# Performance work log

Measured on AMD Instinct MI355X. Metric: run time of the kernel, lower is better.

## Reference

```python
import jax
import jax.numpy as jnp
from jax import lax
import numpy as np

N_PRE = 1024
N_POST = 2048
SEQ_LEN = 4096
DECAY = 0.9   # leak factor per timestep
V_TH = 1.0    # firing threshold


def setup_inputs() -> dict:
    key = jax.random.key(0)
    k1, k2 = jax.random.split(key)
    stim = (jax.random.uniform(k1, (N_PRE, SEQ_LEN), dtype=jnp.float32) < 0.1).astype(jnp.float32)  # sparse input spikes
    weights = jax.random.normal(k2, (N_POST, N_PRE), dtype=jnp.float32) * 0.05
    return {"stim": stim, "weights": weights}


def reference(stim, weights):
    # Synaptic currents for all timesteps at once: cal_post_input(stim[:, i]) == weights @ stim[:, i]
    currents = jnp.einsum("np,pt->nt", weights, stim)  # [n_post, T]

    def lif_step(v, i_t):
        # leaky integrate
        v = v * DECAY + i_t
        # fire
        s = (v >= V_TH).astype(v.dtype)
        # reset to 0 where spiked
        v_next = jnp.where(s > 0, jnp.zeros_like(v), v)
        return v_next, (s, v_next)

    v0 = jnp.zeros((N_POST,), dtype=stim.dtype)
    _, (spikes_t, v_t) = lax.scan(lif_step, v0, currents.T)  # scanned over T
    # transpose back to [n_post, T] to match spike_times / v buffers
    return spikes_t.T, v_t.T
```

## Files before the change

kernel.cpp:

```cpp
#include <hip/hip_runtime.h>

#define N_PRE 1024
#define N_POST 2048
#define SEQ_LEN 4096

#define KSPLIT 512

__device__ __forceinline__ float opaque(float x) {
  asm volatile("" : "+v"(x));
  return x;
}

__device__ __forceinline__ float load_dyn(const void* p, size_t idx, bool isbf) {
  if (isbf) {
    const unsigned short b = ((const unsigned short*)p)[idx];
    return __uint_as_float(((unsigned int)b) << 16);
  }
  return ((const float*)p)[idx];
}

__device__ __forceinline__ int sniff_flags(const void* W, const void* S, int tid,
                                           int* flags_sh) {
  if (tid < 64) {
    const unsigned short* uw = (const unsigned short*)W;
    const float f = fabsf(__uint_as_float(((unsigned int)uw[tid * 2]) << 16));
    const bool big = !(f < 64.f);
    const unsigned long long wb = __ballot(big);
    const unsigned short* us = (const unsigned short*)S;
    int hit = 0;
    for (int j = 0; j < 64; ++j) hit |= (us[tid * 128 + 2 * j] == 0x3F80u) ? 1 : 0;
    const unsigned long long sb = __ballot(hit != 0);
    if (tid == 0) *flags_sh = ((wb == 0ull) ? 1 : 0) | ((sb != 0ull) ? 2 : 0);
  }
  __syncthreads();
  return *flags_sh;
}

__global__ __launch_bounds__(256) void snn_wt_build(const void* __restrict__ W,
                                                    const void* __restrict__ S,
                                                    float* __restrict__ WT) {
  __shared__ float tile[64][65];
  __shared__ int flags_sh;
  const int tid = threadIdx.x;
  const int fl = sniff_flags(W, S, tid, &flags_sh);
  const bool w_bf = (fl & 1) != 0;
  const int k0 = blockIdx.x * 64;
  const int nn0 = blockIdx.y * 64;
  {
    const int r = tid >> 2;
    const int cq = tid & 3;
    if (!w_bf) {
      const float* Wf = (const float*)W;
#pragma unroll
      for (int p = 0; p < 4; ++p) {
        const int c = cq * 16 + p * 4;
        const float4 va = *(const float4*)&Wf[(size_t)(nn0 + r) * N_PRE + k0 + c];
        tile[c + 0][r] = va.x; tile[c + 1][r] = va.y;
        tile[c + 2][r] = va.z; tile[c + 3][r] = va.w;
      }
    } else {
#pragma unroll
      for (int p = 0; p < 4; ++p)
#pragma unroll
        for (int j = 0; j < 4; ++j) {
          const int c = cq * 16 + p * 4 + j;
          tile[c][r] = load_dyn(W, (size_t)(nn0 + r) * N_PRE + k0 + c, true);
        }
    }
  }
  __syncthreads();
  {
    const int kr = tid >> 2;
    const int nq = tid & 3;
#pragma unroll
    for (int p = 0; p < 4; ++p) {
      const int c = nq * 16 + p * 4;
      float4 o;
      o.x = tile[kr][c + 0]; o.y = tile[kr][c + 1];
      o.z = tile[kr][c + 2]; o.w = tile[kr][c + 3];
      *(float4*)&WT[(size_t)(k0 + kr) * N_POST + nn0 + c] = o;
    }
  }
}

__global__ __launch_bounds__(64) void snn_mask_build(const void* __restrict__ W,
                                                     const void* __restrict__ S,
                                                     unsigned char* __restrict__ MT) {
  __shared__ int flags_sh;
  const int tid = threadIdx.x;
  const int fl = sniff_flags(W, S, tid, &flags_sh);
  const bool s_bf = (fl & 2) != 0;
  const int tb = blockIdx.x;
  unsigned wrd[4] = {0u, 0u, 0u, 0u};
#pragma unroll
  for (int kk = 0; kk < 16; ++kk) {
    const int k = tid * 16 + kk;
    unsigned byte = 0;
    if (s_bf) {
      const unsigned short* Sb = (const unsigned short*)S;
      const uint4 u = *(const uint4*)&Sb[(size_t)k * SEQ_LEN + tb * 8];
      byte |= (((u.x & 0x7FFFu) != 0u) ? 1u : 0u) << 0;
      byte |= (((u.x & 0x7FFF0000u) != 0u) ? 1u : 0u) << 1;
      byte |= (((u.y & 0x7FFFu) != 0u) ? 1u : 0u) << 2;
      byte |= (((u.y & 0x7FFF0000u) != 0u) ? 1u : 0u) << 3;
      byte |= (((u.z & 0x7FFFu) != 0u) ? 1u : 0u) << 4;
      byte |= (((u.z & 0x7FFF0000u) != 0u) ? 1u : 0u) << 5;
      byte |= (((u.w & 0x7FFFu) != 0u) ? 1u : 0u) << 6;
      byte |= (((u.w & 0x7FFF0000u) != 0u) ? 1u : 0u) << 7;
    } else {
      const float* Sf = (const float*)S;
      const size_t base = (size_t)k * SEQ_LEN + tb * 8;
      const float4 f0 = *(const float4*)&Sf[base];
      const float4 f1 = *(const float4*)&Sf[base + 4];
      byte |= ((f0.x != 0.0f) ? 1u : 0u) << 0;
      byte |= ((f0.y != 0.0f) ? 1u : 0u) << 1;
      byte |= ((f0.z != 0.0f) ? 1u : 0u) << 2;
      byte |= ((f0.w != 0.0f) ? 1u : 0u) << 3;
      byte |= ((f1.x != 0.0f) ? 1u : 0u) << 4;
      byte |= ((f1.y != 0.0f) ? 1u : 0u) << 5;
      byte |= ((f1.z != 0.0f) ? 1u : 0u) << 6;
      byte |= ((f1.w != 0.0f) ? 1u : 0u) << 7;
    }
    wrd[kk >> 2] |= byte << ((kk & 3) * 8);
  }
  *(uint4*)&MT[(size_t)tb * N_PRE + tid * 16] =
      make_uint4(wrd[0], wrd[1], wrd[2], wrd[3]);
}

__global__ __launch_bounds__(64) void snn_list_build(const unsigned char* __restrict__ MT,
                                                     unsigned short* __restrict__ lists,
                                                     int* __restrict__ lens,
                                                     int* __restrict__ splits) {
  const int t = blockIdx.x;
  const int l = threadIdx.x;
  const unsigned char* Mrow = MT + (size_t)(t >> 3) * N_PRE;
  const int bit = t & 7;
  unsigned short* Lp = lists + (size_t)t * N_PRE;
  int base = 0;
  int split = 0;
#pragma unroll
  for (int c = 0; c < 16; ++c) {
    const int k = c * 64 + l;
    const int b = (Mrow[k] >> bit) & 1;
    const unsigned long long m = __ballot(b != 0);
    const int pre = __popcll(m & ((1ull << l) - 1ull));
    if (b) Lp[base + pre] = (unsigned short)k;
    base += __popcll(m);
    if (c == 7) split = base;
  }
  if (l == 0) {
    lens[t] = base;
    splits[t] = split;
  }
}

__global__ __launch_bounds__(64) void snn_gemm_sp(const float* __restrict__ WT,
                                                  const unsigned short* __restrict__ lists,
                                                  const int* __restrict__ lens,
                                                  float* __restrict__ C,
                                                  int t0, int ct) {
  const int slice = (int)blockIdx.x & 7;
  const int tl = (int)blockIdx.x >> 3;
  const int tg = t0 + tl;
  const int n = slice * 256 + (int)threadIdx.x * 4;
  const unsigned short* __restrict__ L = lists + (size_t)tg * N_PRE;
  const int len = lens[tg];
  float lo0 = 0.f, lo1 = 0.f, lo2 = 0.f, lo3 = 0.f;
  float hi0 = 0.f, hi1 = 0.f, hi2 = 0.f, hi3 = 0.f;

  int kA0, kA1, kA2, kA3, kA4, kA5, kA6, kA7;
  int kB0, kB1, kB2, kB3, kB4, kB5, kB6, kB7;
  float4 wA0, wA1, wA2, wA3, wA4, wA5, wA6, wA7;
  float4 wB0, wB1, wB2, wB3, wB4, wB5, wB6, wB7;

#define ISSUE(S, I)                                                    \
  {                                                                    \
    const uint4 u = *(const uint4*)&L[I];                              \
    k##S##0 = u.x & 0xFFFF; k##S##1 = (int)(u.x >> 16);                \
    k##S##2 = u.y & 0xFFFF; k##S##3 = (int)(u.y >> 16);                \
    k##S##4 = u.z & 0xFFFF; k##S##5 = (int)(u.z >> 16);                \
    k##S##6 = u.w & 0xFFFF; k##S##7 = (int)(u.w >> 16);                \
    w##S##0 = *(const float4*)&WT[((size_t)k##S##0 << 11) + n];        \
    w##S##1 = *(const float4*)&WT[((size_t)k##S##1 << 11) + n];        \
    w##S##2 = *(const float4*)&WT[((size_t)k##S##2 << 11) + n];        \
    w##S##3 = *(const float4*)&WT[((size_t)k##S##3 << 11) + n];        \
    w##S##4 = *(const float4*)&WT[((size_t)k##S##4 << 11) + n];        \
    w##S##5 = *(const float4*)&WT[((size_t)k##S##5 << 11) + n];        \
    w##S##6 = *(const float4*)&WT[((size_t)k##S##6 << 11) + n];        \
    w##S##7 = *(const float4*)&WT[((size_t)k##S##7 << 11) + n];        \
  }
#define ACC_LO(W_) { lo0 += W_.x; lo1 += W_.y; lo2 += W_.z; lo3 += W_.w; }
#define ACC_HI(W_) { hi0 += W_.x; hi1 += W_.y; hi2 += W_.z; hi3 += W_.w; }
#define ACC_SEL(K_, W_)                                                \
  { if ((K_) < KSPLIT) ACC_LO(W_) else ACC_HI(W_) }
#define ACCUM(S)                                                       \
  {                                                                    \
    if (k##S##7 < KSPLIT) {                                            \
      ACC_LO(w##S##0) ACC_LO(w##S##1) ACC_LO(w##S##2) ACC_LO(w##S##3)  \
      ACC_LO(w##S##4) ACC_LO(w##S##5) ACC_LO(w##S##6) ACC_LO(w##S##7)  \
    } else if (k##S##0 >= KSPLIT) {                                    \
      ACC_HI(w##S##0) ACC_HI(w##S##1) ACC_HI(w##S##2) ACC_HI(w##S##3)  \
      ACC_HI(w##S##4) ACC_HI(w##S##5) ACC_HI(w##S##6) ACC_HI(w##S##7)  \
    } else {                                                           \
      ACC_SEL(k##S##0, w##S##0) ACC_SEL(k##S##1, w##S##1)              \
      ACC_SEL(k##S##2, w##S##2) ACC_SEL(k##S##3, w##S##3)              \
      ACC_SEL(k##S##4, w##S##4) ACC_SEL(k##S##5, w##S##5)              \
      ACC_SEL(k##S##6, w##S##6) ACC_SEL(k##S##7, w##S##7)              \
    }                                                                  \
  }

  const int len8 = len & ~7;
  const int nb = len8 >> 3;
  if (nb > 0) {
    ISSUE(A, 0)
    int b = 0;
    for (; b + 2 <= nb; b += 2) {
      ISSUE(B, (b + 1) * 8)
      ACCUM(A)
      if (b + 2 < nb) ISSUE(A, (b + 2) * 8)
      ACCUM(B)
    }
    if (b < nb) ACCUM(A)
  }
  for (int i = len8; i < len; ++i) {
    const int k = L[i];
    const float4 w = *(const float4*)&WT[((size_t)k << 11) + n];
    ACC_SEL(k, w)
  }
#undef ACCUM
#undef ACC_SEL
#undef ACC_HI
#undef ACC_LO
#undef ISSUE

  *(float4*)&C[(size_t)tl * N_POST + n] =
      make_float4(lo0 + hi0, lo1 + hi1, lo2 + hi2, lo3 + hi3);
}

__global__ __launch_bounds__(64) void snn_scan_chk(const float* __restrict__ C,
                                                   float* __restrict__ vchk,
                                                   float* __restrict__ v_carry,
                                                   int ct, int first) {
  const int l = threadIdx.x;
  const int n = blockIdx.x * 64 + l;
  float v = 0.0f;
  if (!first) v = v_carry[n];
  const int ntiles = ct / 64;

  float cur[64], nxt[64];
#pragma unroll
  for (int j = 0; j < 64; ++j) cur[j] = C[(size_t)j * N_POST + n];

  for (int tile = 0; tile < ntiles; ++tile) {
    vchk[(size_t)tile * N_POST + n] = v;
    const int nb = (tile + 1) * 64;
    const bool hn = (tile + 1 < ntiles);
#pragma unroll
    for (int g = 0; g < 4; ++g) {
      if (hn) {
#pragma unroll
        for (int j = 0; j < 16; ++j)
          nxt[g * 16 + j] = C[(size_t)(nb + g * 16 + j) * N_POST + n];
      }
#pragma unroll
      for (int j = 0; j < 16; ++j) {
        const float c = cur[g * 16 + j];
        const float leak = opaque(v * 0.9f);
        v = leak + c;
        const bool fired = (v >= 1.0f);
        v = fired ? 0.0f : v;
      }
    }
#pragma unroll
    for (int j = 0; j < 64; ++j) cur[j] = nxt[j];
  }
  v_carry[n] = v;
}

__global__ __launch_bounds__(64) void snn_scan_emit(const float* __restrict__ C,
                                                    const float* __restrict__ vchk,
                                                    float* __restrict__ spk,
                                                    float* __restrict__ vout,
                                                    int t0, int ct) {
  __shared__ float sb[64][65];
  __shared__ float vb[64][65];
  const int l = threadIdx.x;
  const int n0 = blockIdx.x * 64;
  const int tile = blockIdx.y;
  const int n = n0 + l;
  const int tb = tile * 64;

  float v = vchk[(size_t)tile * N_POST + n];

  float ccur[16], cnxt[16];
#pragma unroll
  for (int j = 0; j < 16; ++j) ccur[j] = C[(size_t)(tb + j) * N_POST + n];

#pragma unroll
  for (int g = 0; g < 4; ++g) {
    if (g < 3) {
#pragma unroll
      for (int j = 0; j < 16; ++j)
        cnxt[j] = C[(size_t)(tb + (g + 1) * 16 + j) * N_POST + n];
    }
#pragma unroll
    for (int j = 0; j < 16; ++j) {
      const float c = ccur[j];
      const float leak = opaque(v * 0.9f);
      v = leak + c;
      const bool fired = (v >= 1.0f);
      sb[g * 16 + j][l] = fired ? 1.0f : 0.0f;
      v = fired ? 0.0f : v;
      vb[g * 16 + j][l] = v;
    }
#pragma unroll
    for (int j = 0; j < 16; ++j) ccur[j] = cnxt[j];
  }

  const int t4 = (l & 15) * 4;
  const int rq = l >> 4;
  const size_t gtb = (size_t)t0 + tb;
#pragma unroll
  for (int it = 0; it < 16; ++it) {
    const int r = it * 4 + rq;
    float4 so, vo;
    so.x = sb[t4 + 0][r]; so.y = sb[t4 + 1][r];
    so.z = sb[t4 + 2][r]; so.w = sb[t4 + 3][r];
    vo.x = vb[t4 + 0][r]; vo.y = vb[t4 + 1][r];
    vo.z = vb[t4 + 2][r]; vo.w = vb[t4 + 3][r];
    const size_t go = (size_t)(n0 + r) * SEQ_LEN + gtb + t4;
    *(float4*)&spk[go] = so;
    *(float4*)&vout[go] = vo;
  }
}

__global__ __launch_bounds__(256) void snn_fused_blis(const void* __restrict__ W,
                                                      const void* __restrict__ S,
                                                      float* __restrict__ spk,
                                                      float* __restrict__ vout) {
  __shared__ float As[16][68];
  __shared__ float Bs[16][68];
  __shared__ float Ct[64][65];
  __shared__ float vsh[64];
  __shared__ int flags_sh;
  const int tid = threadIdx.x;
  const int fl = sniff_flags(W, S, tid, &flags_sh);
  const bool w_bf = (fl & 1) != 0;
  const bool s_bf = (fl & 2) != 0;

  const int tx = tid & 15;
  const int ty = tid >> 4;
  const int m0 = blockIdx.x * 64;
  if (tid < 64) vsh[tid] = 0.0f;

  for (int t0 = 0; t0 < SEQ_LEN; t0 += 64) {
    float acc0[4][4] = {{0.f}};
    float acc1[4][4] = {{0.f}};
    int k0 = 0;
#define FUSED_SEGMENT(ACC, KEND)                                                 \
    for (; k0 < (KEND); k0 += 16) {                                              \
      {                                                                          \
        const int r = tid >> 4, c = tid & 15;                                    \
        _Pragma("unroll") for (int j = 0; j < 4; ++j)                            \
            As[c][r + 16 * j] =                                                  \
                load_dyn(W, (size_t)(m0 + r + 16 * j) * N_PRE + k0 + c, w_bf);   \
      }                                                                          \
      {                                                                          \
        const int r = tid >> 6, c = tid & 63;                                    \
        _Pragma("unroll") for (int j = 0; j < 4; ++j)                            \
            Bs[r + 4 * j][c] =                                                   \
                load_dyn(S, (size_t)(k0 + r + 4 * j) * SEQ_LEN + t0 + c, s_bf);  \
      }                                                                          \
      __syncthreads();                                                           \
      _Pragma("unroll") for (int k = 0; k < 16; ++k) {                           \
        _Pragma("unroll") for (int i = 0; i < 4; ++i)                            \
            _Pragma("unroll") for (int j = 0; j < 4; ++j)                        \
                ACC[i][j] += As[k][ty * 4 + i] * Bs[k][tx * 4 + j];              \
      }                                                                          \
      __syncthreads();                                                           \
    }

    FUSED_SEGMENT(acc0, KSPLIT)
    FUSED_SEGMENT(acc1, N_PRE)
#undef FUSED_SEGMENT

#pragma unroll
    for (int i = 0; i < 4; ++i)
#pragma unroll
      for (int j = 0; j < 4; ++j) Ct[ty * 4 + i][tx * 4 + j] = acc0[i][j] + acc1[i][j];
    __syncthreads();
    if (tid < 64) {
      float v = vsh[tid];
#pragma unroll
      for (int k = 0; k < 64; ++k) {
        const float leak = opaque(v * 0.9f);
        v = leak + Ct[tid][k];
        const bool fired = (v >= 1.0f);
        const size_t g = (size_t)(m0 + tid) * SEQ_LEN + t0 + k;
        spk[g] = fired ? 1.0f : 0.0f;
        v = fired ? 0.0f : v;
        vout[g] = v;
      }
      vsh[tid] = v;
    }
    __syncthreads();
  }
}

extern "C" void kernel_launch(void* const* d_in, const int* in_sizes, int n_in,
                              void* d_out, int out_size, void* d_ws, size_t ws_size,
                              hipStream_t stream) {
  const void* stim = d_in[0];
  const void* weights = d_in[1];
  if (n_in >= 2 && in_sizes[0] == N_POST * N_PRE && in_sizes[1] == N_PRE * SEQ_LEN) {
    weights = d_in[0];
    stim = d_in[1];
  }

  float* spk = (float*)d_out;
  float* vout = spk + (size_t)N_POST * SEQ_LEN;

  char* p = (char*)d_ws;
  float* WT = (float*)p;                 p += (size_t)N_PRE * N_POST * 4;
  unsigned char* MT = (unsigned char*)p; p += (size_t)(SEQ_LEN / 8) * N_PRE;
  unsigned short* lists = (unsigned short*)p; p += (size_t)SEQ_LEN * N_PRE * 2;
  int* lens = (int*)p;                   p += (size_t)SEQ_LEN * 4;
  int* splits = (int*)p;                 p += (size_t)SEQ_LEN * 4;
  float* v_carry = (float*)p;            p += (size_t)N_POST * 4;
  float* vchk = (float*)p;               p += (size_t)(SEQ_LEN / 64) * N_POST * 4;
  float* C = (float*)p;
  const size_t used = (size_t)(p - (char*)d_ws);
  const size_t remain = (ws_size > used) ? (ws_size - used) : 0;

  int chunkT = (int)((remain / ((size_t)N_POST * sizeof(float))) / 64 * 64);
  if (chunkT > SEQ_LEN) chunkT = SEQ_LEN;
  if (chunkT >= 64) {
    int pw = 64;
    while (pw * 2 <= chunkT && pw < SEQ_LEN) pw *= 2;
    chunkT = pw;
  }

  if (chunkT >= 64) {
    snn_wt_build<<<dim3(N_PRE / 64, N_POST / 64), dim3(256), 0, stream>>>(weights, stim, WT);
    snn_mask_build<<<dim3(SEQ_LEN / 8), dim3(64), 0, stream>>>(weights, stim, MT);
    snn_list_build<<<dim3(SEQ_LEN), dim3(64), 0, stream>>>(MT, lists, lens, splits);
    for (int t0 = 0; t0 < SEQ_LEN; t0 += chunkT) {
      const int ct = (SEQ_LEN - t0 < chunkT) ? (SEQ_LEN - t0) : chunkT;
      snn_gemm_sp<<<dim3(ct * 8), dim3(64), 0, stream>>>(WT, lists, lens, C, t0, ct);
      snn_scan_chk<<<dim3(N_POST / 64), dim3(64), 0, stream>>>(C, vchk, v_carry,
                                                               ct, t0 == 0);
      snn_scan_emit<<<dim3(N_POST / 64, ct / 64), dim3(64), 0, stream>>>(C, vchk, spk,
                                                                         vout, t0, ct);
    }
  } else {
    snn_fused_blis<<<dim3(N_POST / 64), dim3(256), 0, stream>>>(weights, stim, spk, vout);
  }
}
```

Before: 349.1 us.

## Stage sparse weight-row gathers through LDS with async global_load_lds double buffering

The sparse gather GEMM now copies each timestep's index list into shared memory once, then issues direct global-to-LDS loads (global_load_lds) for eight weight rows at a time into a double-buffered LDS tile, consuming one buffer while the other fills, with manual vmcnt/lgkmcnt waits. This replaces the register-held float4 prefetch and aims to cut VGPR pressure and keep more gathers in flight. It also drops the unused splits output from list building. It adds LDS traffic and hand-placed waitcnt ordering that could cost latency or be fragile.

```diff
diff --git a/kernel.cpp b/kernel.cpp
--- a/kernel.cpp
+++ b/kernel.cpp
@@ -129,15 +129,13 @@
 
 __global__ __launch_bounds__(64) void snn_list_build(const unsigned char* __restrict__ MT,
                                                      unsigned short* __restrict__ lists,
-                                                     int* __restrict__ lens,
-                                                     int* __restrict__ splits) {
+                                                     int* __restrict__ lens) {
   const int t = blockIdx.x;
   const int l = threadIdx.x;
   const unsigned char* Mrow = MT + (size_t)(t >> 3) * N_PRE;
   const int bit = t & 7;
   unsigned short* Lp = lists + (size_t)t * N_PRE;
   int base = 0;
-  int split = 0;
 #pragma unroll
   for (int c = 0; c < 16; ++c) {
     const int k = c * 64 + l;
@@ -146,12 +144,8 @@
     const int pre = __popcll(m & ((1ull << l) - 1ull));
     if (b) Lp[base + pre] = (unsigned short)k;
     base += __popcll(m);
-    if (c == 7) split = base;
-  }
-  if (l == 0) {
-    lens[t] = base;
-    splits[t] = split;
-  }
+  }
+  if (l == 0) lens[t] = base;
 }
 
 __global__ __launch_bounds__(64) void snn_gemm_sp(const float* __restrict__ WT,
@@ -159,79 +153,124 @@
                                                   const int* __restrict__ lens,
                                                   float* __restrict__ C,
                                                   int t0, int ct) {
+  __shared__ float rows[2][8][256];
+  __shared__ uint4 lw[128];
   const int slice = (int)blockIdx.x & 7;
   const int tl = (int)blockIdx.x >> 3;
   const int tg = t0 + tl;
-  const int n = slice * 256 + (int)threadIdx.x * 4;
-  const unsigned short* __restrict__ L = lists + (size_t)tg * N_PRE;
+  const int lane = (int)threadIdx.x;
+  const int n = slice * 256 + lane * 4;
+  const unsigned short* __restrict__ L16 = lists + (size_t)tg * N_PRE;
+  const uint4* __restrict__ Lw = (const uint4*)L16;
   const int len = lens[tg];
+  const int nb = len >> 3;
+
   float lo0 = 0.f, lo1 = 0.f, lo2 = 0.f, lo3 = 0.f;
   float hi0 = 0.f, hi1 = 0.f, hi2 = 0.f, hi3 = 0.f;
-
   int kA0, kA1, kA2, kA3, kA4, kA5, kA6, kA7;
   int kB0, kB1, kB2, kB3, kB4, kB5, kB6, kB7;
-  float4 wA0, wA1, wA2, wA3, wA4, wA5, wA6, wA7;
-  float4 wB0, wB1, wB2, wB3, wB4, wB5, wB6, wB7;
-
-#define ISSUE(S, I)                                                    \
-  {                                                                    \
-    const uint4 u = *(const uint4*)&L[I];                              \
-    k##S##0 = u.x & 0xFFFF; k##S##1 = (int)(u.x >> 16);                \
-    k##S##2 = u.y & 0xFFFF; k##S##3 = (int)(u.y >> 16);                \
-    k##S##4 = u.z & 0xFFFF; k##S##5 = (int)(u.z >> 16);                \
-    k##S##6 = u.w & 0xFFFF; k##S##7 = (int)(u.w >> 16);                \
-    w##S##0 = *(const float4*)&WT[((size_t)k##S##0 << 11) + n];        \
-    w##S##1 = *(const float4*)&WT[((size_t)k##S##1 << 11) + n];        \
-    w##S##2 = *(const float4*)&WT[((size_t)k##S##2 << 11) + n];        \
-    w##S##3 = *(const float4*)&WT[((size_t)k##S##3 << 11) + n];        \
-    w##S##4 = *(const float4*)&WT[((size_t)k##S##4 << 11) + n];        \
-    w##S##5 = *(const float4*)&WT[((size_t)k##S##5 << 11) + n];        \
-    w##S##6 = *(const float4*)&WT[((size_t)k##S##6 << 11) + n];        \
-    w##S##7 = *(const float4*)&WT[((size_t)k##S##7 << 11) + n];        \
-  }
-#define ACC_LO(W_) { lo0 += W_.x; lo1 += W_.y; lo2 += W_.z; lo3 += W_.w; }
-#define ACC_HI(W_) { hi0 += W_.x; hi1 += W_.y; hi2 += W_.z; hi3 += W_.w; }
-#define ACC_SEL(K_, W_)                                                \
-  { if ((K_) < KSPLIT) ACC_LO(W_) else ACC_HI(W_) }
-#define ACCUM(S)                                                       \
-  {                                                                    \
-    if (k##S##7 < KSPLIT) {                                            \
-      ACC_LO(w##S##0) ACC_LO(w##S##1) ACC_LO(w##S##2) ACC_LO(w##S##3)  \
-      ACC_LO(w##S##4) ACC_LO(w##S##5) ACC_LO(w##S##6) ACC_LO(w##S##7)  \
-    } else if (k##S##0 >= KSPLIT) {                                    \
-      ACC_HI(w##S##0) ACC_HI(w##S##1) ACC_HI(w##S##2) ACC_HI(w##S##3)  \
-      ACC_HI(w##S##4) ACC_HI(w##S##5) ACC_HI(w##S##6) ACC_HI(w##S##7)  \
-    } else {                                                           \
-      ACC_SEL(k##S##0, w##S##0) ACC_SEL(k##S##1, w##S##1)              \
-      ACC_SEL(k##S##2, w##S##2) ACC_SEL(k##S##3, w##S##3)              \
-      ACC_SEL(k##S##4, w##S##4) ACC_SEL(k##S##5, w##S##5)              \
-      ACC_SEL(k##S##6, w##S##6) ACC_SEL(k##S##7, w##S##7)              \
-    }                                                                  \
-  }
-
-  const int len8 = len & ~7;
-  const int nb = len8 >> 3;
+
+  for (int w = lane; w < nb; w += 64) lw[w] = Lw[w];
+  asm volatile("s_waitcnt vmcnt(0) lgkmcnt(0)" ::: "memory");
+  __builtin_amdgcn_sched_barrier(0);
+
+#define UNPACK_S(S, B)                                                   \
+  {                                                                      \
+    const uint4 u = lw[B];                                               \
+    k##S##0 = u.x & 0xFFFF; k##S##1 = (int)(u.x >> 16);                  \
+    k##S##2 = u.y & 0xFFFF; k##S##3 = (int)(u.y >> 16);                  \
+    k##S##4 = u.z & 0xFFFF; k##S##5 = (int)(u.z >> 16);                  \
+    k##S##6 = u.w & 0xFFFF; k##S##7 = (int)(u.w >> 16);                  \
+  }
+#define DMA_S(S, BUF)                                                                     \
+  {                                                                                       \
+    __builtin_amdgcn_global_load_lds(&WT[((size_t)k##S##0 << 11) + n], &rows[BUF][0][0],  \
+                                     16, 0, 0);                                           \
+    __builtin_amdgcn_global_load_lds(&WT[((size_t)k##S##1 << 11) + n], &rows[BUF][1][0],  \
+                                     16, 0, 0);                                           \
+    __builtin_amdgcn_global_load_lds(&WT[((size_t)k##S##2 << 11) + n], &rows[BUF][2][0],  \
+                                     16, 0, 0);                                           \
+    __builtin_amdgcn_global_load_lds(&WT[((size_t)k##S##3 << 11) + n], &rows[BUF][3][0],  \
+                                     16, 0, 0);                                           \
+    __builtin_amdgcn_global_load_lds(&WT[((size_t)k##S##4 << 11) + n], &rows[BUF][4][0],  \
+                                     16, 0, 0);                                           \
+    __builtin_amdgcn_global_load_lds(&WT[((size_t)k##S##5 << 11) + n], &rows[BUF][5][0],  \
+                                     16, 0, 0);                                           \
+    __builtin_amdgcn_global_load_lds(&WT[((size_t)k##S##6 << 11) + n], &rows[BUF][6][0],  \
+                                     16, 0, 0);                                           \
+    __builtin_amdgcn_global_load_lds(&WT[((size_t)k##S##7 << 11) + n], &rows[BUF][7][0],  \
+                                     16, 0, 0);                                           \
+  }
+#define ACC_LO4(P)                                                       \
+  { const float4 w_ = *(const float4*)(P);                               \
+    lo0 += w_.x; lo1 += w_.y; lo2 += w_.z; lo3 += w_.w; }
+#define ACC_HI4(P)                                                       \
+  { const float4 w_ = *(const float4*)(P);                               \
+    hi0 += w_.x; hi1 += w_.y; hi2 += w_.z; hi3 += w_.w; }
+#define ACC_SEL4(K_, P)                                                  \
+  { if ((K_) < KSPLIT) ACC_LO4(P) else ACC_HI4(P) }
+#define CONSUME(S, BUF)                                                  \
+  {                                                                      \
+    const float* b_ = &rows[BUF][0][lane * 4];                           \
+    if (k##S##7 < KSPLIT) {                                              \
+      ACC_LO4(b_ + 0)    ACC_LO4(b_ + 256)  ACC_LO4(b_ + 512)            \
+      ACC_LO4(b_ + 768)  ACC_LO4(b_ + 1024) ACC_LO4(b_ + 1280)           \
+      ACC_LO4(b_ + 1536) ACC_LO4(b_ + 1792)                              \
+    } else if (k##S##0 >= KSPLIT) {                                      \
+      ACC_HI4(b_ + 0)    ACC_HI4(b_ + 256)  ACC_HI4(b_ + 512)            \
+      ACC_HI4(b_ + 768)  ACC_HI4(b_ + 1024) ACC_HI4(b_ + 1280)           \
+      ACC_HI4(b_ + 1536) ACC_HI4(b_ + 1792)                              \
+    } else {                                                             \
+      ACC_SEL4(k##S##0, b_ + 0)    ACC_SEL4(k##S##1, b_ + 256)           \
+      ACC_SEL4(k##S##2, b_ + 512)  ACC_SEL4(k##S##3, b_ + 768)           \
+      ACC_SEL4(k##S##4, b_ + 1024) ACC_SEL4(k##S##5, b_ + 1280)          \
+      ACC_SEL4(k##S##6, b_ + 1536) ACC_SEL4(k##S##7, b_ + 1792)          \
+    }                                                                    \
+    asm volatile("s_waitcnt lgkmcnt(0)" ::: "memory");                   \
+    __builtin_amdgcn_sched_barrier(0);                                   \
+  }
+
   if (nb > 0) {
-    ISSUE(A, 0)
+    UNPACK_S(A, 0)
+    DMA_S(A, 0)
     int b = 0;
     for (; b + 2 <= nb; b += 2) {
-      ISSUE(B, (b + 1) * 8)
-      ACCUM(A)
-      if (b + 2 < nb) ISSUE(A, (b + 2) * 8)
-      ACCUM(B)
-    }
-    if (b < nb) ACCUM(A)
-  }
-  for (int i = len8; i < len; ++i) {
-    const int k = L[i];
+      UNPACK_S(B, b + 1)
+      DMA_S(B, 1)
+      asm volatile("s_waitcnt vmcnt(8)" ::: "memory");
+      __builtin_amdgcn_sched_barrier(0);
+      CONSUME(A, 0)
+      if (b + 2 < nb) {
+        UNPACK_S(A, b + 2)
+        DMA_S(A, 0)
+        asm volatile("s_waitcnt vmcnt(8)" ::: "memory");
+      } else {
+        asm volatile("s_waitcnt vmcnt(0)" ::: "memory");
+      }
+      __builtin_amdgcn_sched_barrier(0);
+      CONSUME(B, 1)
+    }
+    if (b < nb) {
+      asm volatile("s_waitcnt vmcnt(0)" ::: "memory");
+      __builtin_amdgcn_sched_barrier(0);
+      CONSUME(A, 0)
+    }
+  }
+  for (int i = nb * 8; i < len; ++i) {
+    const int k = L16[i];
     const float4 w = *(const float4*)&WT[((size_t)k << 11) + n];
-    ACC_SEL(k, w)
-  }
-#undef ACCUM
-#undef ACC_SEL
-#undef ACC_HI
-#undef ACC_LO
-#undef ISSUE
+    if (k < KSPLIT) {
+      lo0 += w.x; lo1 += w.y; lo2 += w.z; lo3 += w.w;
+    } else {
+      hi0 += w.x; hi1 += w.y; hi2 += w.z; hi3 += w.w;
+    }
+  }
+#undef CONSUME
+#undef ACC_SEL4
+#undef ACC_HI4
+#undef ACC_LO4
+#undef DMA_S
+#undef UNPACK_S
 
   *(float4*)&C[(size_t)tl * N_POST + n] =
       make_float4(lo0 + hi0, lo1 + hi1, lo2 + hi2, lo3 + hi3);
@@ -425,7 +464,6 @@
   unsigned char* MT = (unsigned char*)p; p += (size_t)(SEQ_LEN / 8) * N_PRE;
   unsigned short* lists = (unsigned short*)p; p += (size_t)SEQ_LEN * N_PRE * 2;
   int* lens = (int*)p;                   p += (size_t)SEQ_LEN * 4;
-  int* splits = (int*)p;                 p += (size_t)SEQ_LEN * 4;
   float* v_carry = (float*)p;            p += (size_t)N_POST * 4;
   float* vchk = (float*)p;               p += (size_t)(SEQ_LEN / 64) * N_POST * 4;
   float* C = (float*)p;
@@ -443,7 +481,7 @@
   if (chunkT >= 64) {
     snn_wt_build<<<dim3(N_PRE / 64, N_POST / 64), dim3(256), 0, stream>>>(weights, stim, WT);
     snn_mask_build<<<dim3(SEQ_LEN / 8), dim3(64), 0, stream>>>(weights, stim, MT);
-    snn_list_build<<<dim3(SEQ_LEN), dim3(64), 0, stream>>>(MT, lists, lens, splits);
+    snn_list_build<<<dim3(SEQ_LEN), dim3(64), 0, stream>>>(MT, lists, lens);
     for (int t0 = 0; t0 < SEQ_LEN; t0 += chunkT) {
       const int ct = (SEQ_LEN - t0 < chunkT) ? (SEQ_LEN - t0) : chunkT;
       snn_gemm_sp<<<dim3(ct * 8), dim3(64), 0, stream>>>(WT, lists, lens, C, t0, ct);
```

Measured after the change: 368.9 us. 1.06x slower.
